# Kernel optimization log

Hardware: AMD Instinct MI355X
Metric: run time of the kernel (lower is better)

The kernel has to match this reference:

```python
import jax, jax.numpy as jnp
import numpy as np

NUM_HEADS = 16
HEAD_DIM = 64  # att_output_dim // num_heads = 1024 // 16


def setup_inputs() -> dict:
    key = jax.random.key(0)
    ks = jax.random.split(key, 7)
    B, S, D_IN, D_OUT = 4, 2048, 1024, 1024
    std = 1.0 / np.sqrt(D_IN)
    return {
        "ts10_input": jax.random.normal(ks[0], (B, S, D_IN), dtype=jnp.float32),
        "Wq": jax.random.uniform(ks[1], (D_IN, D_OUT), jnp.float32, -std, std),
        "bq": jax.random.uniform(ks[2], (D_OUT,), jnp.float32, -std, std),
        "Wk": jax.random.uniform(ks[3], (D_IN, D_OUT), jnp.float32, -std, std),
        "bk": jax.random.uniform(ks[4], (D_OUT,), jnp.float32, -std, std),
        "Wv": jax.random.uniform(ks[5], (D_IN, D_OUT), jnp.float32, -std, std),
        "bv": jax.random.uniform(ks[6], (D_OUT,), jnp.float32, -std, std),
        "mask": 1,
    }


def reference(ts10_input, Wq, bq, Wk, bk, Wv, bv, mask):
    B, S, _ = ts10_input.shape
    H, Dh = NUM_HEADS, HEAD_DIM

    def split_heads(x):  # (B,S,H*Dh) -> (B,H,S,Dh)
        return x.reshape(B, S, H, Dh).transpose(0, 2, 1, 3)

    q = split_heads(ts10_input @ Wq + bq)
    k = split_heads(ts10_input @ Wk + bk)
    v = split_heads(ts10_input @ Wv + bv)

    scores = jnp.einsum("bhqd,bhkd->bhqk", q, k) / jnp.sqrt(jnp.float32(Dh))
    if mask:
        causal = jnp.tril(jnp.ones((S, S), dtype=bool))  # keep lower triangle incl diag
        scores = jnp.where(causal, scores, -jnp.inf)
    probs = jax.nn.softmax(scores, axis=-1)
    ctx = jnp.einsum("bhqk,bhkd->bhqd", probs, v)
    return ctx.transpose(0, 2, 1, 3).reshape(B, S, H * Dh)
```

## Files before the change

### kernel.cpp

```cpp
#include <hip/hip_runtime.h>

typedef __bf16 bf16x8 __attribute__((ext_vector_type(8)));
typedef __bf16 bf16x4 __attribute__((ext_vector_type(4)));
typedef short s16x4 __attribute__((ext_vector_type(4)));
typedef float f32x4 __attribute__((ext_vector_type(4)));
typedef unsigned short u16x8 __attribute__((ext_vector_type(8)));
typedef unsigned short u16x4 __attribute__((ext_vector_type(4)));
typedef unsigned int u32x2 __attribute__((ext_vector_type(2)));
typedef unsigned int __attribute__((address_space(1))) as1_uint;
typedef unsigned int __attribute__((address_space(3))) as3_uint;

#define S_LEN 2048
#define NB 4
#define NH 16
#define HD 64
#define DM 1024

#define Q_SCALE 0.18033688011112042f

__device__ __forceinline__ unsigned short f2bf(float f) {
  union { float f; unsigned int u; } v; v.f = f;
  unsigned int r = v.u + 0x7fffu + ((v.u >> 16) & 1u);
  return (unsigned short)(r >> 16);
}

__device__ __forceinline__ unsigned int fbits(float f) {
  union { float f; unsigned int u; } v; v.f = f;
  return v.u;
}

__device__ __forceinline__ f32x4 mfma16(u16x4 a, u16x4 b, f32x4 c) {
#if __has_builtin(__builtin_amdgcn_mfma_f32_16x16x16_bf16)
  return __builtin_amdgcn_mfma_f32_16x16x16_bf16(
      __builtin_bit_cast(bf16x4, a), __builtin_bit_cast(bf16x4, b), c, 0, 0, 0);
#else
  return __builtin_amdgcn_mfma_f32_16x16x16bf16_1k(
      __builtin_bit_cast(s16x4, a), __builtin_bit_cast(s16x4, b), c, 0, 0, 0);
#endif
}

__global__ __launch_bounds__(256) void cvt_all(const float* __restrict__ x,
                                               unsigned short* __restrict__ xb,
                                               const float* __restrict__ Wq,
                                               const float* __restrict__ Wk,
                                               const float* __restrict__ Wv,
                                               unsigned short* __restrict__ wt) {
  __shared__ float tile[32][33];
  const int bid = blockIdx.x;
  if (bid < 4096) {
    int i = (bid * 256 + threadIdx.x) * 8;
    f32x4 a = *(const f32x4*)(x + i);
    f32x4 b = *(const f32x4*)(x + i + 4);
    u16x8 o;
    o[0] = f2bf(a[0]); o[1] = f2bf(a[1]); o[2] = f2bf(a[2]); o[3] = f2bf(a[3]);
    o[4] = f2bf(b[0]); o[5] = f2bf(b[1]); o[6] = f2bf(b[2]); o[7] = f2bf(b[3]);
    *(u16x8*)(xb + i) = o;
  } else {
    const int r = bid - 4096;
    const int z = r >> 10;
    const int rr = r & 1023;
    const float* W = (z == 0) ? Wq : (z == 1) ? Wk : Wv;
    unsigned short* WT = wt + (size_t)z * DM * DM;
    int tx = threadIdx.x & 31, ty = threadIdx.x >> 5;
    int k0 = (rr & 31) * 32, n0 = (rr >> 5) * 32;
#pragma unroll
    for (int i = 0; i < 4; ++i)
      tile[ty + 8 * i][tx] = W[(size_t)(k0 + ty + 8 * i) * DM + n0 + tx];
    __syncthreads();
#pragma unroll
    for (int i = 0; i < 4; ++i)
      WT[(size_t)(n0 + ty + 8 * i) * DM + k0 + tx] = f2bf(tile[tx][ty + 8 * i]);
  }
}

#define QKV_LDS_BYTES 147456
__global__ __launch_bounds__(512, 2) void qkv_gemm(const unsigned short* __restrict__ xb,
                                                   const unsigned short* __restrict__ wt,
                                                   const float* __restrict__ bq,
                                                   const float* __restrict__ bk,
                                                   const float* __restrict__ bv,
                                                   unsigned short* __restrict__ qo,
                                                   unsigned short* __restrict__ ko,
                                                   unsigned short* __restrict__ vto) {
  extern __shared__ char smem_dyn[];
  unsigned short* As = (unsigned short*)smem_dyn;
  unsigned short* Bs = As + 3 * 256 * 64;
  const int z = blockIdx.z;
  const unsigned short* WT = wt + (size_t)z * DM * DM;
  const float* bias = (z == 0) ? bq : (z == 1) ? bk : bv;
  const int m0 = blockIdx.x * 256;
  const int n0 = blockIdx.y * 128;
  const int tid = threadIdx.x;
  const int wave = tid >> 6, lane = tid & 63, quad = lane >> 4, lw = lane & 15;
  const int wm = (wave >> 1) * 64, wn = (wave & 1) * 64;

  f32x4 acc[4][4];
#pragma unroll
  for (int mt = 0; mt < 4; ++mt)
#pragma unroll
    for (int nt = 0; nt < 4; ++nt) acc[mt][nt] = (f32x4){0.f, 0.f, 0.f, 0.f};

  auto stage = [&](int tile) {
    const int kt = tile * 64;
    const int bsel = tile % 3;
    unsigned short* Ad = As + bsel * (256 * 64);
    unsigned short* Bd = Bs + bsel * (128 * 64);
#pragma unroll
    for (int i = 0; i < 4; ++i) {
      int c = i * 512 + tid;
      int row = c >> 3, scn = (c & 7) ^ (row & 7);
      __builtin_amdgcn_global_load_lds((const as1_uint*)(xb + (size_t)(m0 + row) * DM + kt + scn * 8),
                                       (as3_uint*)(Ad + c * 8), 16, 0, 0);
    }
#pragma unroll
    for (int i = 0; i < 2; ++i) {
      int c = i * 512 + tid;
      int row = c >> 3, scn = (c & 7) ^ (row & 7);
      __builtin_amdgcn_global_load_lds((const as1_uint*)(WT + (size_t)(n0 + row) * DM + kt + scn * 8),
                                       (as3_uint*)(Bd + c * 8), 16, 0, 0);
    }
  };

  stage(0);
  stage(1);
  asm volatile("s_waitcnt vmcnt(6)" ::: "memory");
  __builtin_amdgcn_s_barrier();
  asm volatile("" ::: "memory");

#pragma unroll
  for (int t = 0; t < 16; ++t) {
    if (t + 2 < 16) stage(t + 2);

    const unsigned short* Ab = As + (t % 3) * (256 * 64);
    const unsigned short* Bb = Bs + (t % 3) * (128 * 64);
    bf16x8 af[2][4], bfq[2][4];
#pragma unroll
    for (int k = 0; k < 2; ++k) {
#pragma unroll
      for (int mt = 0; mt < 4; ++mt) {
        int r = wm + mt * 16 + lw;
        af[k][mt] = *(const bf16x8*)(Ab + r * 64 + (((k * 4 + quad) ^ (r & 7)) * 8));
      }
#pragma unroll
      for (int nt = 0; nt < 4; ++nt) {
        int r = wn + nt * 16 + lw;
        bfq[k][nt] = *(const bf16x8*)(Bb + r * 64 + (((k * 4 + quad) ^ (r & 7)) * 8));
      }
    }
#pragma unroll
    for (int k = 0; k < 2; ++k)
#pragma unroll
      for (int mt = 0; mt < 4; ++mt)
#pragma unroll
        for (int nt = 0; nt < 4; ++nt)
          acc[mt][nt] = __builtin_amdgcn_mfma_f32_16x16x32_bf16(af[k][mt], bfq[k][nt], acc[mt][nt], 0, 0, 0);

    if (t < 15) {
      if (t < 14) asm volatile("s_waitcnt vmcnt(6)" ::: "memory");
      else        asm volatile("s_waitcnt vmcnt(0)" ::: "memory");
      __builtin_amdgcn_s_barrier();
      asm volatile("" ::: "memory");
    }
  }

  float bias4[4];
#pragma unroll
  for (int nt = 0; nt < 4; ++nt) bias4[nt] = bias[n0 + wn + nt * 16 + lw];

  if (z < 2) {
    unsigned short* dst = (z == 0) ? qo : ko;
    const float sc = (z == 0) ? Q_SCALE : 1.0f;
#pragma unroll
    for (int mt = 0; mt < 4; ++mt) {
#pragma unroll
      for (int nt = 0; nt < 4; ++nt) {
        int n = n0 + wn + nt * 16 + lw;
        int h = n >> 6, d = n & 63;
#pragma unroll
        for (int r = 0; r < 4; ++r) {
          int m = m0 + wm + mt * 16 + quad * 4 + r;
          int b = m >> 11, s = m & 2047;
          dst[((size_t)(b * NH + h) * S_LEN + s) * HD + d] = f2bf((acc[mt][nt][r] + bias4[nt]) * sc);
        }
      }
    }
  } else {
#pragma unroll
    for (int mt = 0; mt < 4; ++mt) {
#pragma unroll
      for (int nt = 0; nt < 4; ++nt) {
        int n = n0 + wn + nt * 16 + lw;
        int h = n >> 6, d = n & 63;
        int mb = m0 + wm + mt * 16 + quad * 4;
        int b = mb >> 11, s = mb & 2047;
        u16x4 pk;
#pragma unroll
        for (int r = 0; r < 4; ++r) pk[r] = f2bf(acc[mt][nt][r] + bias4[nt]);
        int u = s >> 2;
        int us = ((u & ~15) | ((u & 15) ^ (d & 15))) << 2;
        *(u16x4*)(vto + ((size_t)(b * NH + h) * HD + d) * S_LEN + us) = pk;
      }
    }
  }
}

__global__ __launch_bounds__(256, 5) void attn(const unsigned short* __restrict__ Qb,
                                               const unsigned short* __restrict__ Kb,
                                               const unsigned short* __restrict__ Vtb,
                                               float* __restrict__ out) {
  const int flat = blockIdx.x;
  const int bh_lo = flat & 7;
  const int rest = flat >> 3;
  const int qidx = 31 - (rest >> 3);
  const int bh_hi = rest & 7;
  const int bh = bh_lo | (bh_hi << 3);
  const int b = bh >> 4, h = bh & 15;
  const int tid = threadIdx.x;
  const int wave = tid >> 6, lane = tid & 63;
  const int quad = lane >> 4, lw = lane & 15;
  const unsigned short* Qp = Qb + (size_t)bh * S_LEN * HD;
  const unsigned short* Kp = Kb + (size_t)bh * S_LEN * HD;
  const unsigned short* Vp = Vtb + (size_t)bh * HD * S_LEN;

  __shared__ __align__(16) unsigned short Kl[2][64 * 64];
  __shared__ __align__(16) unsigned short Vl[2][64 * 64];

  const int qbase = qidx * 64;
  bf16x8 aq[2];
#pragma unroll
  for (int kc = 0; kc < 2; ++kc)
    aq[kc] = *(const bf16x8*)(Qp + (size_t)(qbase + wave * 16 + lw) * HD + kc * 32 + quad * 8);

  u16x4 ones4;
#pragma unroll
  for (int i = 0; i < 4; ++i) ones4[i] = 0x3F80;

  f32x4 accO[4];
  f32x4 accL = (f32x4){0.f, 0.f, 0.f, 0.f};
#pragma unroll
  for (int dg = 0; dg < 4; ++dg) accO[dg] = (f32x4){0.f, 0.f, 0.f, 0.f};

  const int qr = qbase + wave * 16 + lw;
  const int T = qidx + 1;
  const int swk = (lw & 7) ^ (((lw >> 3) & 1) << 2);

#pragma unroll
  for (int i = 0; i < 2; ++i) {
    int idx = i * 256 + tid;
    int r = idx >> 3;
    int ck = (idx & 7) ^ (r & 7) ^ (((r >> 3) & 1) << 2);
    __builtin_amdgcn_global_load_lds((const as1_uint*)(Kp + (size_t)r * HD + ck * 8),
                                     (as3_uint*)(Kl[0] + idx * 8), 16, 0, 0);
    __builtin_amdgcn_global_load_lds((const as1_uint*)(Vp + (size_t)r * S_LEN + (idx & 7) * 8),
                                     (as3_uint*)(Vl[0] + idx * 8), 16, 0, 0);
  }

  for (int t = 0; t < T; ++t) {
    const int kv = t * 64;
    const int cur = t & 1;
    __syncthreads();

    if (t + 1 < T) {
      const int kvn = kv + 64;
#pragma unroll
      for (int i = 0; i < 2; ++i) {
        int idx = i * 256 + tid;
        int r = idx >> 3;
        int ck = (idx & 7) ^ (r & 7) ^ (((r >> 3) & 1) << 2);
        __builtin_amdgcn_global_load_lds((const as1_uint*)(Kp + (size_t)(kvn + r) * HD + ck * 8),
                                         (as3_uint*)(Kl[cur ^ 1] + idx * 8), 16, 0, 0);
        __builtin_amdgcn_global_load_lds((const as1_uint*)(Vp + (size_t)r * S_LEN + kvn + (idx & 7) * 8),
                                         (as3_uint*)(Vl[cur ^ 1] + idx * 8), 16, 0, 0);
      }
    }

    const bool diag = (t == qidx);
    __builtin_amdgcn_s_setprio(1);
#pragma unroll
    for (int g = 0; g < 4; ++g) {
      const unsigned short* kp = Kl[cur] + (g * 16 + lw) * 64;
      const int c0 = quad ^ swk;
      bf16x8 kf0 = *(const bf16x8*)(kp + (c0 * 8));
      bf16x8 kf1 = *(const bf16x8*)(kp + ((c0 ^ 4) * 8));

      f32x4 s = (f32x4){0.f, 0.f, 0.f, 0.f};
      s = __builtin_amdgcn_mfma_f32_16x16x32_bf16(kf0, aq[0], s, 0, 0, 0);
      s = __builtin_amdgcn_mfma_f32_16x16x32_bf16(kf1, aq[1], s, 0, 0, 0);
      if (diag) {
#pragma unroll
        for (int r = 0; r < 4; ++r) {
          float e = __builtin_amdgcn_exp2f(s[r]);
          s[r] = (kv + g * 16 + quad * 4 + r > qr) ? 0.f : e;
        }
      } else {
#pragma unroll
        for (int r = 0; r < 4; ++r) s[r] = __builtin_amdgcn_exp2f(s[r]);
      }
      u32x2 pk;
      pk[0] = (fbits(s[1]) & 0xFFFF0000u) | (fbits(s[0]) >> 16);
      pk[1] = (fbits(s[3]) & 0xFFFF0000u) | (fbits(s[2]) >> 16);
      u16x4 pf = __builtin_bit_cast(u16x4, pk);

      const int p8 = (4 * g + quad) ^ lw;
#pragma unroll
      for (int dg = 0; dg < 4; ++dg) {
        u16x4 vf = *(const u16x4*)(Vl[cur] + (dg * 16 + lw) * 64 + p8 * 4);
        accO[dg] = mfma16(pf, vf, accO[dg]);
      }
      accL = mfma16(pf, ones4, accL);
    }
    __builtin_amdgcn_s_setprio(0);
  }

  float* op = out + ((size_t)b * S_LEN + qbase + wave * 16 + quad * 4) * DM + h * HD + lw;
#pragma unroll
  for (int r = 0; r < 4; ++r) {
    float inv = 1.0f / accL[r];
#pragma unroll
    for (int dg = 0; dg < 4; ++dg) op[(size_t)r * DM + dg * 16] = accO[dg][r] * inv;
  }
}

extern "C" void kernel_launch(void* const* d_in, const int* in_sizes, int n_in,
                              void* d_out, int out_size, void* d_ws, size_t ws_size,
                              hipStream_t stream) {
  const float* x = (const float*)d_in[0];
  const float* Wq = (const float*)d_in[1];
  const float* bq = (const float*)d_in[2];
  const float* Wk = (const float*)d_in[3];
  const float* bk = (const float*)d_in[4];
  const float* Wv = (const float*)d_in[5];
  const float* bv = (const float*)d_in[6];
  float* out = (float*)d_out;

  char* ws = (char*)d_ws;
  unsigned short* xb = (unsigned short*)(ws + 0);
  unsigned short* wt = (unsigned short*)(ws + 16777216);
  unsigned short* qb = (unsigned short*)(ws + 23068672);
  unsigned short* kb = (unsigned short*)(ws + 39845888);
  unsigned short* vt = (unsigned short*)(ws + 56623104);

  static bool qkv_attr_once = []() {
    hipFuncSetAttribute((const void*)qkv_gemm,
                        hipFuncAttributeMaxDynamicSharedMemorySize, QKV_LDS_BYTES);
    return true;
  }();
  (void)qkv_attr_once;

  hipLaunchKernelGGL(cvt_all, dim3(7168), dim3(256), 0, stream, x, xb, Wq, Wk, Wv, wt);
  hipLaunchKernelGGL(qkv_gemm, dim3(32, 8, 3), dim3(512), QKV_LDS_BYTES, stream,
                     xb, wt, bq, bk, bv, qb, kb, vt);
  hipLaunchKernelGGL(attn, dim3(2048), dim3(256), 0, stream, qb, kb, vt, out);
}
```

Before: 204.1 us.

## Use 16x16x32 MFMA for PV with new K/V LDS swizzle and peeled diagonal tile

Replaces the 16x16x16 bf16 MFMA for the P·V and row-sum products with 16x16x32. It processes two 16-key groups per step, packing the score fragments into an 8-wide bf16 operand. The V transpose layout and the K staging permutation are reworked so the wider fragments come from LDS with 16-byte reads. The loop is unrolled by two with compile-time buffer indices, and the masked diagonal tile is peeled out so the main loop carries no mask branch. This halves the MFMA issue count in the PV stage at the cost of more complex index arithmetic and higher register pressure.

```diff
diff --git a/kernel.cpp b/kernel.cpp
--- a/kernel.cpp
+++ b/kernel.cpp
@@ -7,6 +7,7 @@
 typedef unsigned short u16x8 __attribute__((ext_vector_type(8)));
 typedef unsigned short u16x4 __attribute__((ext_vector_type(4)));
 typedef unsigned int u32x2 __attribute__((ext_vector_type(2)));
+typedef unsigned int u32x4 __attribute__((ext_vector_type(4)));
 typedef unsigned int __attribute__((address_space(1))) as1_uint;
 typedef unsigned int __attribute__((address_space(3))) as3_uint;
 
@@ -29,14 +30,8 @@
   return v.u;
 }
 
-__device__ __forceinline__ f32x4 mfma16(u16x4 a, u16x4 b, f32x4 c) {
-#if __has_builtin(__builtin_amdgcn_mfma_f32_16x16x16_bf16)
-  return __builtin_amdgcn_mfma_f32_16x16x16_bf16(
-      __builtin_bit_cast(bf16x4, a), __builtin_bit_cast(bf16x4, b), c, 0, 0, 0);
-#else
-  return __builtin_amdgcn_mfma_f32_16x16x16bf16_1k(
-      __builtin_bit_cast(s16x4, a), __builtin_bit_cast(s16x4, b), c, 0, 0, 0);
-#endif
+__device__ __forceinline__ f32x4 mfma32(bf16x8 a, bf16x8 b, f32x4 c) {
+  return __builtin_amdgcn_mfma_f32_16x16x32_bf16(a, b, c, 0, 0, 0);
 }
 
 __global__ __launch_bounds__(256) void cvt_all(const float* __restrict__ x,
@@ -196,8 +191,7 @@
         u16x4 pk;
 #pragma unroll
         for (int r = 0; r < 4; ++r) pk[r] = f2bf(acc[mt][nt][r] + bias4[nt]);
-        int u = s >> 2;
-        int us = ((u & ~15) | ((u & 15) ^ (d & 15))) << 2;
+        int us = (s & ~63) | ((((s >> 3) & 7) ^ (d & 7)) << 3) | (s & 7);
         *(u16x4*)(vto + ((size_t)(b * NH + h) * HD + d) * S_LEN + us) = pk;
       }
     }
@@ -231,9 +225,10 @@
   for (int kc = 0; kc < 2; ++kc)
     aq[kc] = *(const bf16x8*)(Qp + (size_t)(qbase + wave * 16 + lw) * HD + kc * 32 + quad * 8);
 
-  u16x4 ones4;
-#pragma unroll
-  for (int i = 0; i < 4; ++i) ones4[i] = 0x3F80;
+  u16x8 one8u;
+#pragma unroll
+  for (int i = 0; i < 8; ++i) one8u[i] = 0x3F80;
+  const bf16x8 ones8 = __builtin_bit_cast(bf16x8, one8u);
 
   f32x4 accO[4];
   f32x4 accL = (f32x4){0.f, 0.f, 0.f, 0.f};
@@ -242,75 +237,101 @@
 
   const int qr = qbase + wave * 16 + lw;
   const int T = qidx + 1;
-  const int swk = (lw & 7) ^ (((lw >> 3) & 1) << 2);
-
+
+  const int c0 = (quad ^ (lw & 7)) * 8;
+  int w8[2];
+#pragma unroll
+  for (int gp = 0; gp < 2; ++gp) w8[gp] = ((gp * 4 + quad) ^ (lw & 7)) * 8;
+
+  int kOff[2], vOff[2], dOff[2];
 #pragma unroll
   for (int i = 0; i < 2; ++i) {
     int idx = i * 256 + tid;
-    int r = idx >> 3;
-    int ck = (idx & 7) ^ (r & 7) ^ (((r >> 3) & 1) << 2);
-    __builtin_amdgcn_global_load_lds((const as1_uint*)(Kp + (size_t)r * HD + ck * 8),
-                                     (as3_uint*)(Kl[0] + idx * 8), 16, 0, 0);
-    __builtin_amdgcn_global_load_lds((const as1_uint*)(Vp + (size_t)r * S_LEN + (idx & 7) * 8),
-                                     (as3_uint*)(Vl[0] + idx * 8), 16, 0, 0);
-  }
-
-  for (int t = 0; t < T; ++t) {
+    int p = idx >> 3;
+    int gsrc = (p & 32) | (((p >> 2) & 3) << 3) | (((p >> 4) & 1) << 2) | (p & 3);
+    int ck = (idx & 7) ^ (p & 7);
+    kOff[i] = gsrc * HD + ck * 8;
+    vOff[i] = p * S_LEN + (idx & 7) * 8;
+    dOff[i] = idx * 8;
+  }
+
+  auto stage = [&](int kvn, int buf) {
+#pragma unroll
+    for (int i = 0; i < 2; ++i) {
+      __builtin_amdgcn_global_load_lds((const as1_uint*)(Kp + (size_t)kvn * HD + kOff[i]),
+                                       (as3_uint*)(&Kl[buf][dOff[i]]), 16, 0, 0);
+      __builtin_amdgcn_global_load_lds((const as1_uint*)(Vp + (size_t)kvn + vOff[i]),
+                                       (as3_uint*)(&Vl[buf][dOff[i]]), 16, 0, 0);
+    }
+  };
+
+  auto body = [&](int t, int cur, bool mask, bool pref) {
     const int kv = t * 64;
-    const int cur = t & 1;
     __syncthreads();
-
-    if (t + 1 < T) {
-      const int kvn = kv + 64;
-#pragma unroll
-      for (int i = 0; i < 2; ++i) {
-        int idx = i * 256 + tid;
-        int r = idx >> 3;
-        int ck = (idx & 7) ^ (r & 7) ^ (((r >> 3) & 1) << 2);
-        __builtin_amdgcn_global_load_lds((const as1_uint*)(Kp + (size_t)(kvn + r) * HD + ck * 8),
-                                         (as3_uint*)(Kl[cur ^ 1] + idx * 8), 16, 0, 0);
-        __builtin_amdgcn_global_load_lds((const as1_uint*)(Vp + (size_t)r * S_LEN + kvn + (idx & 7) * 8),
-                                         (as3_uint*)(Vl[cur ^ 1] + idx * 8), 16, 0, 0);
-      }
-    }
-
-    const bool diag = (t == qidx);
+    if (pref) stage(kv + 64, cur ^ 1);
+
+    const unsigned short* kb = Kl[cur] + lw * 64;
+    const unsigned short* vb = Vl[cur] + lw * 64;
     __builtin_amdgcn_s_setprio(1);
 #pragma unroll
-    for (int g = 0; g < 4; ++g) {
-      const unsigned short* kp = Kl[cur] + (g * 16 + lw) * 64;
-      const int c0 = quad ^ swk;
-      bf16x8 kf0 = *(const bf16x8*)(kp + (c0 * 8));
-      bf16x8 kf1 = *(const bf16x8*)(kp + ((c0 ^ 4) * 8));
-
-      f32x4 s = (f32x4){0.f, 0.f, 0.f, 0.f};
-      s = __builtin_amdgcn_mfma_f32_16x16x32_bf16(kf0, aq[0], s, 0, 0, 0);
-      s = __builtin_amdgcn_mfma_f32_16x16x32_bf16(kf1, aq[1], s, 0, 0, 0);
-      if (diag) {
+    for (int gp = 0; gp < 2; ++gp) {
+      const unsigned short* kg = kb + gp * 2048;
+      bf16x8 k00 = *(const bf16x8*)(kg + c0);
+      bf16x8 k01 = *(const bf16x8*)(kg + (c0 ^ 32));
+      bf16x8 k10 = *(const bf16x8*)(kg + 1024 + c0);
+      bf16x8 k11 = *(const bf16x8*)(kg + 1024 + (c0 ^ 32));
+
+      f32x4 s0 = (f32x4){0.f, 0.f, 0.f, 0.f};
+      f32x4 s1 = (f32x4){0.f, 0.f, 0.f, 0.f};
+      s0 = mfma32(k00, aq[0], s0);
+      s0 = mfma32(k01, aq[1], s0);
+      s1 = mfma32(k10, aq[0], s1);
+      s1 = mfma32(k11, aq[1], s1);
+
+      if (mask) {
+        const int kvb = kv + gp * 32 + 8 * quad;
 #pragma unroll
         for (int r = 0; r < 4; ++r) {
-          float e = __builtin_amdgcn_exp2f(s[r]);
-          s[r] = (kv + g * 16 + quad * 4 + r > qr) ? 0.f : e;
+          float e0 = __builtin_amdgcn_exp2f(s0[r]);
+          float e1 = __builtin_amdgcn_exp2f(s1[r]);
+          s0[r] = (kvb + r > qr) ? 0.f : e0;
+          s1[r] = (kvb + 4 + r > qr) ? 0.f : e1;
         }
       } else {
 #pragma unroll
-        for (int r = 0; r < 4; ++r) s[r] = __builtin_amdgcn_exp2f(s[r]);
-      }
-      u32x2 pk;
-      pk[0] = (fbits(s[1]) & 0xFFFF0000u) | (fbits(s[0]) >> 16);
-      pk[1] = (fbits(s[3]) & 0xFFFF0000u) | (fbits(s[2]) >> 16);
-      u16x4 pf = __builtin_bit_cast(u16x4, pk);
-
-      const int p8 = (4 * g + quad) ^ lw;
+        for (int r = 0; r < 4; ++r) {
+          s0[r] = __builtin_amdgcn_exp2f(s0[r]);
+          s1[r] = __builtin_amdgcn_exp2f(s1[r]);
+        }
+      }
+      u32x4 pw;
+      pw[0] = (fbits(s0[1]) & 0xFFFF0000u) | (fbits(s0[0]) >> 16);
+      pw[1] = (fbits(s0[3]) & 0xFFFF0000u) | (fbits(s0[2]) >> 16);
+      pw[2] = (fbits(s1[1]) & 0xFFFF0000u) | (fbits(s1[0]) >> 16);
+      pw[3] = (fbits(s1[3]) & 0xFFFF0000u) | (fbits(s1[2]) >> 16);
+      bf16x8 af = __builtin_bit_cast(bf16x8, pw);
+
 #pragma unroll
       for (int dg = 0; dg < 4; ++dg) {
-        u16x4 vf = *(const u16x4*)(Vl[cur] + (dg * 16 + lw) * 64 + p8 * 4);
-        accO[dg] = mfma16(pf, vf, accO[dg]);
-      }
-      accL = mfma16(pf, ones4, accL);
+        bf16x8 vf = *(const bf16x8*)(vb + dg * 1024 + w8[gp]);
+        accO[dg] = mfma32(af, vf, accO[dg]);
+      }
+      accL = mfma32(af, ones8, accL);
     }
     __builtin_amdgcn_s_setprio(0);
-  }
+  };
+
+  stage(0, 0);
+
+  int t = 0;
+  const int nmain = T - 1;
+  for (; t + 1 < nmain; t += 2) {
+    body(t, 0, false, true);
+    body(t + 1, 1, false, true);
+  }
+  if (t < nmain) { body(t, 0, false, true); ++t; }
+  if (t & 1) body(t, 1, true, false);
+  else       body(t, 0, true, false);
 
   float* op = out + ((size_t)b * S_LEN + qbase + wave * 16 + quad * 4) * DM + h * HD + lw;
 #pragma unroll
```

Result: no change. 200.9 us (-1.6%).
